# Optimization experiments

Measured on AMD Instinct MI355X. Metric: run time of the kernel, lower is better.

The kernel has to match this reference:

```python
import jax, jax.numpy as jnp
import numpy as np

B, S, E, H = 4, 1024, 1024, 16
D = E // H          # head_dim = 64
ROT = 32            # rotary dims (first ROT channels of each head)


def _rope(x, freqs):
    # x: [B, H, S, D]; freqs: [1, 1, S, ROT]
    r = freqs.shape[-1]
    xl, xr = x[..., :r], x[..., r:]
    half = r // 2
    rot = jnp.concatenate([-xl[..., half:], xl[..., :half]], axis=-1)  # rotate_half
    xl = xl * jnp.cos(freqs) + rot * jnp.sin(freqs)
    return jnp.concatenate([xl, xr], axis=-1)


def setup_inputs() -> dict:
    key = jax.random.key(0)
    ks = jax.random.split(key, 7)
    std = 0.02
    return {
        "hidden_states": jax.random.normal(ks[0], (B, S, E), jnp.float32),
        "rotary_pos_emb": jax.random.normal(ks[1], (1, S, ROT), jnp.float32),
        "q_w": jax.random.normal(ks[2], (E, E), jnp.float32) * std,
        "k_w": jax.random.normal(ks[3], (E, E), jnp.float32) * std,
        "v_w": jax.random.normal(ks[4], (E, E), jnp.float32) * std,
        "o_w": jax.random.normal(ks[5], (E, E), jnp.float32) * std,
        "o_b": jnp.zeros((E,), jnp.float32),
    }


def reference(hidden_states, rotary_pos_emb, q_w, k_w, v_w, o_w, o_b):
    bsz, tgt_len, embed_dim = hidden_states.shape
    scale = D ** -0.5

    def shape(t):  # [B, S, E] -> [B, H, S, D]
        return t.reshape(bsz, tgt_len, H, D).transpose(0, 2, 1, 3)

    q = shape(hidden_states @ q_w.T * scale)
    k = shape(hidden_states @ k_w.T)
    v = shape(hidden_states @ v_w.T)

    freqs = rotary_pos_emb[:, None, :, :]  # [1, 1, S, ROT]
    q = _rope(q, freqs)
    k = _rope(k, freqs)
    v = _rope(v, freqs)

    attn = jnp.einsum("bhqd,bhkd->bhqk", q, k)
    causal = jnp.tril(jnp.ones((tgt_len, tgt_len), bool))
    attn = jnp.where(causal, attn, jnp.finfo(attn.dtype).min)
    attn = jax.nn.softmax(attn, axis=-1)

    out = jnp.einsum("bhqk,bhkd->bhqd", attn, v)
    out = out.transpose(0, 2, 1, 3).reshape(bsz, tgt_len, embed_dim)
    return out @ o_w.T + o_b
```

## Files before the change

### kernel.cpp

```cpp
#include <hip/hip_runtime.h>
#include <hip/hip_bf16.h>

typedef __bf16 bf16;
typedef __attribute__((ext_vector_type(2))) __bf16 bf16x2;
typedef __attribute__((ext_vector_type(4))) __bf16 bf16x4;
typedef __attribute__((ext_vector_type(8))) __bf16 bf16x8;
typedef __attribute__((ext_vector_type(4))) float f32x4;

#define NB 4
#define NS 1024
#define NE 1024
#define NH 16
#define ND 64
#define NROT 32
#define NM (NB*NS)

__device__ __forceinline__ void gload_lds16(const bf16* g, void* l) {
  __builtin_amdgcn_global_load_lds(
      (const __attribute__((address_space(1))) unsigned int*)g,
      (__attribute__((address_space(3))) unsigned int*)l,
      16, 0, 0);
}

struct PrepArgs {
  const float* w0; const float* w1; const float* w2; const float* w3;
  bf16* b0; bf16* b1; bf16* b2; bf16* b3;
  const float* hs; bf16* hb;
  const float* rot; float* ct; float* st;
};
__global__ void k_prep(PrepArgs a) {
  const int y = blockIdx.y;
  const int i = blockIdx.x * 256 + threadIdx.x;
  if (y < 4) {
    const float* s = (y == 0) ? a.w0 : (y == 1) ? a.w1 : (y == 2) ? a.w2 : a.w3;
    bf16* d = (y == 0) ? a.b0 : (y == 1) ? a.b1 : (y == 2) ? a.b2 : a.b3;
    float4 v = reinterpret_cast<const float4*>(s)[i];
    bf16x4 o = { (bf16)v.x, (bf16)v.y, (bf16)v.z, (bf16)v.w };
    *reinterpret_cast<bf16x4*>(d + (size_t)i * 4) = o;
  } else if (y < 8) {
    size_t off = (size_t)(y - 4) * (NM * NE / 16);
    float4 v = reinterpret_cast<const float4*>(a.hs)[off + i];
    bf16x4 o = { (bf16)v.x, (bf16)v.y, (bf16)v.z, (bf16)v.w };
    *reinterpret_cast<bf16x4*>(a.hb + (off + i) * 4) = o;
  } else {
    if (i < NS * NROT) {
      float v = a.rot[i];
      a.ct[i] = cosf(v);
      a.st[i] = sinf(v);
    }
  }
}

template<int BM, int BN, bool SWAP>
__device__ __forceinline__ void gemm_core(
    const bf16* __restrict__ A, const bf16* __restrict__ W,
    bf16* lA, bf16* lB, int m0, int n0, f32x4 (&acc)[BM/32][BN/32])
{
  const int tid = threadIdx.x;
  const int wave = tid >> 6, lane = tid & 63;
  const int wm = wave >> 1, wn = wave & 1;
  const int fr = lane & 15, kg = lane >> 4;

  const int sline = lane >> 3;
  const int lsl   = (lane & 7) ^ sline;
  const int srow  = 2 * sline + (lsl >> 2);
  const int skcol = (lsl & 3) * 8;
  constexpr int ACH = BM / 64;
  constexpr int BCH = BN / 64;
  constexpr int NSTAGE = ACH + BCH;

  auto stage = [&](int kt, int c) {
#pragma unroll
    for (int i = 0; i < ACH; ++i) {
      int chunk = i * 4 + wave;
      gload_lds16(A + (size_t)(m0 + chunk * 16 + srow) * NE + kt + skcol,
                  (char*)lA + c * (BM * 64) + chunk * 1024);
    }
#pragma unroll
    for (int i = 0; i < BCH; ++i) {
      int chunk = i * 4 + wave;
      gload_lds16(W + (size_t)(n0 + chunk * 16 + srow) * NE + kt + skcol,
                  (char*)lB + c * (BN * 64) + chunk * 1024);
    }
  };

  auto foff = [&](int ra) {
    return (ra >> 1) * 128 + (((((ra & 1) << 2) + kg) ^ ((ra >> 1) & 7)) << 4);
  };

  stage(0, 0);

  for (int kt = 0; kt < NE / 32; ++kt) {
    const int c = kt & 1;
    if (kt + 1 < NE / 32) {
      stage((kt + 1) * 32, c ^ 1);
      asm volatile("s_waitcnt vmcnt(%0)\n\ts_barrier" :: "n"(NSTAGE) : "memory");
    } else {
      asm volatile("s_waitcnt vmcnt(0)\n\ts_barrier" ::: "memory");
    }

    const char* cA = (const char*)lA + c * (BM * 64);
    const char* cB = (const char*)lB + c * (BN * 64);
    bf16x8 af[BM / 32], bfr[BN / 32];
#pragma unroll
    for (int i = 0; i < BM / 32; ++i)
      af[i] = *reinterpret_cast<const bf16x8*>(cA + foff(wm * (BM / 2) + i * 16 + fr));
#pragma unroll
    for (int j = 0; j < BN / 32; ++j)
      bfr[j] = *reinterpret_cast<const bf16x8*>(cB + foff(wn * (BN / 2) + j * 16 + fr));
#pragma unroll
    for (int i = 0; i < BM / 32; ++i)
#pragma unroll
      for (int j = 0; j < BN / 32; ++j) {
        if constexpr (SWAP)
          acc[j][i] = __builtin_amdgcn_mfma_f32_16x16x32_bf16(bfr[j], af[i], acc[j][i], 0, 0, 0);
        else
          acc[i][j] = __builtin_amdgcn_mfma_f32_16x16x32_bf16(af[i], bfr[j], acc[i][j], 0, 0, 0);
      }
    asm volatile("s_waitcnt lgkmcnt(0)\n\ts_barrier" ::: "memory");
  }
}

__global__ __launch_bounds__(256) void k_proj(
    const bf16* __restrict__ A, const bf16* __restrict__ Wq, const bf16* __restrict__ Wk,
    const bf16* __restrict__ Wv, bf16* __restrict__ Oq, bf16* __restrict__ Ok,
    bf16* __restrict__ vt, const float* __restrict__ ct, const float* __restrict__ st)
{
  __shared__ bf16 lA[2 * 128 * 32];
  __shared__ bf16 lB[2 * 128 * 32];
  const int z = blockIdx.z;
  const int m0 = blockIdx.x * 128, n0 = blockIdx.y * 128;
  const int tid = threadIdx.x;
  const int wave = tid >> 6, lane = tid & 63;
  const int wm = wave >> 1, wn = wave & 1;
  const int fr = lane & 15, kg = lane >> 4;

  if (z == 2) {
    f32x4 acc[4][4] = {};
    gemm_core<128, 128, true>(A, Wv, lA, lB, m0, n0, acc);

    const int b = m0 >> 10;
    const int h = (n0 + wn * 64) >> 6;
    bf16* vtb = vt + ((size_t)(b * 16 + h)) * ND * NS;
#pragma unroll
    for (int i = 0; i < 4; ++i) {
      int sl = (m0 & (NS - 1)) + wm * 64 + i * 16 + fr;
#pragma unroll
      for (int r = 0; r < 4; ++r) {
        int dbase = kg * 4 + r;
        float x0 = acc[0][i][r];
        float x1 = acc[1][i][r];
        float c0 = ct[sl * NROT + dbase],      sn0 = st[sl * NROT + dbase];
        float c1 = ct[sl * NROT + 16 + dbase], sn1 = st[sl * NROT + 16 + dbase];
        float y0 = x0 * c0 - x1 * sn0;
        float y1 = x1 * c1 + x0 * sn1;
        vtb[(size_t)(dbase)      * NS + sl] = (bf16)y0;
        vtb[(size_t)(16 + dbase) * NS + sl] = (bf16)y1;
        vtb[(size_t)(32 + dbase) * NS + sl] = (bf16)acc[2][i][r];
        vtb[(size_t)(48 + dbase) * NS + sl] = (bf16)acc[3][i][r];
      }
    }
  } else {
    const bf16* W = (z == 0) ? Wq : Wk;
    bf16* Og = (z == 0) ? Oq : Ok;
    const float scale = (z == 0) ? 0.125f * 1.44269504f : 1.0f;

    f32x4 acc[4][4] = {};
    gemm_core<128, 128, false>(A, W, lA, lB, m0, n0, acc);

#pragma unroll
    for (int i = 0; i < 4; ++i) {
      int rowbase = m0 + wm * 64 + i * 16 + kg * 4;
#pragma unroll
      for (int r = 0; r < 4; ++r) {
        int gm = rowbase + r;
        int s = gm & (NS - 1);
        float x0 = acc[i][0][r] * scale;
        float x1 = acc[i][1][r] * scale;
        float c0 = ct[s * NROT + fr],      sn0 = st[s * NROT + fr];
        float c1 = ct[s * NROT + 16 + fr], sn1 = st[s * NROT + 16 + fr];
        float y0 = x0 * c0 - x1 * sn0;
        float y1 = x1 * c1 + x0 * sn1;
        size_t rb = (size_t)gm * NE + n0 + wn * 64;
        Og[rb + 0 * 16 + fr] = (bf16)y0;
        Og[rb + 1 * 16 + fr] = (bf16)y1;
        Og[rb + 2 * 16 + fr] = (bf16)(acc[i][2][r] * scale);
        Og[rb + 3 * 16 + fr] = (bf16)(acc[i][3][r] * scale);
      }
    }
  }
}

__global__ __launch_bounds__(256) void k_gemm_o(
    const bf16* __restrict__ A, const bf16* __restrict__ W, float* __restrict__ Og,
    const float* __restrict__ bias)
{
  __shared__ bf16 lA[2 * 64 * 32];
  __shared__ bf16 lB[2 * 128 * 32];
  const int m0 = blockIdx.x * 64, n0 = blockIdx.y * 128;
  f32x4 acc[2][4] = {};
  gemm_core<64, 128, false>(A, W, lA, lB, m0, n0, acc);

  const int tid = threadIdx.x;
  const int wave = tid >> 6, lane = tid & 63;
  const int wm = wave >> 1, wn = wave & 1;
  const int fr = lane & 15, kg = lane >> 4;
#pragma unroll
  for (int i = 0; i < 2; ++i)
#pragma unroll
    for (int j = 0; j < 4; ++j) {
      int gc = n0 + wn * 64 + j * 16 + fr;
      float bv = bias[gc];
#pragma unroll
      for (int r = 0; r < 4; ++r) {
        int gm = m0 + wm * 32 + i * 16 + kg * 4 + r;
        Og[(size_t)gm * NE + gc] = acc[i][j][r] + bv;
      }
    }
}

__global__ __launch_bounds__(256) void k_attn(
    const bf16* __restrict__ Q, const bf16* __restrict__ K,
    const bf16* __restrict__ VT, bf16* __restrict__ O)
{
  __shared__ bf16 lK[2][64 * 64];
  __shared__ bf16 lVT[64 * 64];
  __shared__ bf16 lP[4][16 * 68];
  const int tid = threadIdx.x;
  const int wave = tid >> 6, lane = tid & 63;
  const int fr = lane & 15, kg = lane >> 4;

  const int qt = 15 - (blockIdx.y >> 3);
  const int bh = blockIdx.x | ((blockIdx.y & 7) << 3);
  const int b = bh >> 4, h = bh & 15;
  const int nt = qt + 1;
  const bf16* Qb  = Q + (size_t)b * NS * NE + h * 64;
  const bf16* Kb  = K + (size_t)b * NS * NE + h * 64;
  const bf16* VTb = VT + (size_t)bh * ND * NS;
  bf16* Ob = O + (size_t)b * NS * NE + h * 64;

  const int qrow0 = qt * 64 + wave * 16;

  bf16x8 qf[2];
#pragma unroll
  for (int kk = 0; kk < 2; ++kk)
    qf[kk] = *reinterpret_cast<const bf16x8*>(
        Qb + (size_t)(qrow0 + fr) * NE + kk * 32 + kg * 8);

  const int srow = lane >> 3;
  const int sslot = (lane & 7) ^ srow;
  const int r0 = wave * 8 + srow;
  const int r1 = (wave + 4) * 8 + srow;
  const bf16* kA0 = Kb + (size_t)r0 * NE + sslot * 8;
  const bf16* kA1 = Kb + (size_t)r1 * NE + sslot * 8;
  const bf16* vA0 = VTb + (size_t)r0 * NS + sslot * 8;
  const bf16* vA1 = VTb + (size_t)r1 * NS + sslot * 8;
  char* ldsKa[2] = { (char*)lK[0] + wave * 1024, (char*)lK[1] + wave * 1024 };
  char* ldsKb[2] = { (char*)lK[0] + (wave + 4) * 1024, (char*)lK[1] + (wave + 4) * 1024 };
  char* ldsVa  = (char*)lVT + wave * 1024;
  char* ldsVb  = (char*)lVT + (wave + 4) * 1024;

  float m_ = -3.0e38f, l_ = 0.f;
  f32x4 oacc[4] = {};

  gload_lds16(kA0, ldsKa[0]);
  gload_lds16(kA1, ldsKb[0]);
  __syncthreads();

  for (int t = 0; t < nt; ++t) {
    const int c = t & 1;
    gload_lds16(vA0 + t * 64, ldsVa);
    gload_lds16(vA1 + t * 64, ldsVb);
    if (t + 1 < nt) {
      gload_lds16(kA0 + (size_t)(t + 1) * 64 * NE, ldsKa[c ^ 1]);
      gload_lds16(kA1 + (size_t)(t + 1) * 64 * NE, ldsKb[c ^ 1]);
    }

    const bf16* lKc = lK[c];
    f32x4 sacc[4] = {};
    __builtin_amdgcn_s_setprio(1);
#pragma unroll
    for (int kk = 0; kk < 2; ++kk)
#pragma unroll
      for (int j = 0; j < 4; ++j) {
        int rc = j * 16 + fr;
        bf16x8 kf = *reinterpret_cast<const bf16x8*>(
            lKc + rc * 64 + (((kg + 4 * kk) ^ (rc & 7)) << 3));
        sacc[j] = __builtin_amdgcn_mfma_f32_16x16x32_bf16(kf, qf[kk], sacc[j], 0, 0, 0);
      }
    __builtin_amdgcn_s_setprio(0);

    if (t == qt) {
      const int ql = wave * 16 + fr;
#pragma unroll
      for (int j = 0; j < 4; ++j)
#pragma unroll
        for (int r = 0; r < 4; ++r)
          if (16 * j + 4 * kg + r > ql) sacc[j][r] = -3.0e38f;
    }

    float m4 = fmaxf(fmaxf(fmaxf(sacc[0][0], sacc[0][1]), fmaxf(sacc[0][2], sacc[0][3])),
                     fmaxf(fmaxf(sacc[1][0], sacc[1][1]), fmaxf(sacc[1][2], sacc[1][3])));
    m4 = fmaxf(m4, fmaxf(fmaxf(fmaxf(sacc[2][0], sacc[2][1]), fmaxf(sacc[2][2], sacc[2][3])),
                         fmaxf(fmaxf(sacc[3][0], sacc[3][1]), fmaxf(sacc[3][2], sacc[3][3]))));
    m4 = fmaxf(m4, __shfl_xor(m4, 16));
    m4 = fmaxf(m4, __shfl_xor(m4, 32));

    if (!__all(m4 - m_ <= 8.0f)) {
      float nm = fmaxf(m_, m4);
      float corr = exp2f(m_ - nm);
      m_ = nm;
      l_ *= corr;
#pragma unroll
      for (int r = 0; r < 4; ++r) {
        float cr = __shfl(corr, kg * 4 + r);
#pragma unroll
        for (int df = 0; df < 4; ++df) oacc[df][r] *= cr;
      }
    }

    float ps = 0.f;
#pragma unroll
    for (int j = 0; j < 4; ++j) {
      float p0 = exp2f(sacc[j][0] - m_);
      float p1 = exp2f(sacc[j][1] - m_);
      float p2 = exp2f(sacc[j][2] - m_);
      float p3 = exp2f(sacc[j][3] - m_);
      ps += (p0 + p1) + (p2 + p3);
      bf16x4 pp = { (bf16)p0, (bf16)p1, (bf16)p2, (bf16)p3 };
      *reinterpret_cast<bf16x4*>(&lP[wave][fr * 68 + j * 16 + kg * 4]) = pp;
    }
    ps += __shfl_xor(ps, 16);
    ps += __shfl_xor(ps, 32);
    l_ += ps;

    __syncthreads();

    __builtin_amdgcn_s_setprio(1);
#pragma unroll
    for (int ks = 0; ks < 2; ++ks) {
      bf16x8 pf = *reinterpret_cast<const bf16x8*>(&lP[wave][fr * 68 + ks * 32 + kg * 8]);
#pragma unroll
      for (int df = 0; df < 4; ++df) {
        int d = df * 16 + fr;
        bf16x8 vf = *reinterpret_cast<const bf16x8*>(
            (const bf16*)lVT + d * 64 + (((kg + 4 * ks) ^ (d & 7)) << 3));
        oacc[df] = __builtin_amdgcn_mfma_f32_16x16x32_bf16(pf, vf, oacc[df], 0, 0, 0);
      }
    }
    __builtin_amdgcn_s_setprio(0);

    __syncthreads();
  }

  float linv[4];
#pragma unroll
  for (int r = 0; r < 4; ++r) linv[r] = 1.0f / __shfl(l_, kg * 4 + r);
#pragma unroll
  for (int df = 0; df < 4; ++df)
#pragma unroll
    for (int r = 0; r < 4; ++r)
      Ob[(size_t)(qrow0 + kg * 4 + r) * NE + df * 16 + fr] = (bf16)(oacc[df][r] * linv[r]);
}

extern "C" void kernel_launch(void* const* d_in, const int* in_sizes, int n_in,
                              void* d_out, int out_size, void* d_ws, size_t ws_size,
                              hipStream_t stream) {
  const float* hs  = (const float*)d_in[0];
  const float* rot = (const float*)d_in[1];
  const float* qw  = (const float*)d_in[2];
  const float* kw  = (const float*)d_in[3];
  const float* vw  = (const float*)d_in[4];
  const float* ow  = (const float*)d_in[5];
  const float* obb = (const float*)d_in[6];
  float* out = (float*)d_out;

  char* ws = (char*)d_ws;
  size_t off = 0;
  bf16* hb  = (bf16*)(ws + off); off += (size_t)NM * NE * 2;
  bf16* wqb = (bf16*)(ws + off); off += (size_t)NE * NE * 2;
  bf16* wkb = (bf16*)(ws + off); off += (size_t)NE * NE * 2;
  bf16* wvb = (bf16*)(ws + off); off += (size_t)NE * NE * 2;
  bf16* wob = (bf16*)(ws + off); off += (size_t)NE * NE * 2;
  bf16* qb  = (bf16*)(ws + off); off += (size_t)NM * NE * 2;
  bf16* kb  = (bf16*)(ws + off); off += (size_t)NM * NE * 2;
  bf16* vt  = (bf16*)(ws + off); off += (size_t)NM * NE * 2;
  float* ct = (float*)(ws + off); off += (size_t)NS * NROT * 4;
  float* st = (float*)(ws + off); off += (size_t)NS * NROT * 4;
  bf16* aob = hb;

  PrepArgs pa = { qw, kw, vw, ow, wqb, wkb, wvb, wob, hs, hb, rot, ct, st };
  k_prep<<<dim3(NE * NE / 4 / 256, 9), dim3(256), 0, stream>>>(pa);

  k_proj<<<dim3(NM / 128, NE / 128, 3), dim3(256), 0, stream>>>(
      hb, wqb, wkb, wvb, qb, kb, vt, ct, st);

  k_attn<<<dim3(8, 128), dim3(256), 0, stream>>>(qb, kb, vt, aob);

  k_gemm_o<<<dim3(NM / 64, NE / 128), dim3(256), 0, stream>>>(aob, wob, out, obb);

  (void)in_sizes; (void)n_in; (void)out_size; (void)ws_size;
}
```

Before: 111.7 us.

## Use 256x256 tiles with 8 waves and BK=64 in QKV projection GEMM

Rewrites the QKV projection kernel to use a 256x256 output tile, 512 threads (8 waves in a 2x4 layout), and a K-step of 64 with an XOR-swizzled LDS layout. Each wave now computes a 128x64 sub-tile with 32 accumulators, which raises arithmetic intensity per LDS and global load. The cost is more registers, 128KB of LDS per block, and a grid of only 192 blocks, which may underfill the 256 CUs.

```diff
diff --git a/kernel.cpp b/kernel.cpp
--- a/kernel.cpp
+++ b/kernel.cpp
@@ -51,7 +51,141 @@
   }
 }
 
-template<int BM, int BN, bool SWAP>
+template<bool SWAP>
+__device__ __forceinline__ void gemm_core256(
+    const bf16* __restrict__ A, const bf16* __restrict__ W,
+    bf16* lA, bf16* lB, int m0, int n0, f32x4 (&acc)[32])
+{
+  const int tid = threadIdx.x;
+  const int wave = tid >> 6, lane = tid & 63;
+  const int wm = wave >> 2, wn = wave & 3;
+  const int fr = lane & 15, kg = lane >> 4;
+  const int lrow8 = lane >> 3, lslot = lane & 7;
+
+  auto stage = [&](int kt, int c) {
+#pragma unroll
+    for (int i = 0; i < 4; ++i) {
+      int chunk = i * 8 + wave;
+      int row = (chunk << 3) + lrow8;
+      int slot = lslot ^ (row & 7);
+      gload_lds16(A + (size_t)(m0 + row) * NE + kt + slot * 8,
+                  (char*)lA + c * 32768 + chunk * 1024);
+      gload_lds16(W + (size_t)(n0 + row) * NE + kt + slot * 8,
+                  (char*)lB + c * 32768 + chunk * 1024);
+    }
+  };
+
+  stage(0, 0);
+
+  for (int kt = 0; kt < NE / 64; ++kt) {
+    const int c = kt & 1;
+    if (kt + 1 < NE / 64) {
+      stage((kt + 1) * 64, c ^ 1);
+      asm volatile("s_waitcnt vmcnt(8)\n\ts_barrier" ::: "memory");
+    } else {
+      asm volatile("s_waitcnt vmcnt(0)\n\ts_barrier" ::: "memory");
+    }
+
+    const char* cA = (const char*)lA + c * 32768;
+    const char* cB = (const char*)lB + c * 32768;
+#pragma unroll
+    for (int kk = 0; kk < 2; ++kk) {
+      bf16x8 af[8], bfr[4];
+#pragma unroll
+      for (int i = 0; i < 8; ++i) {
+        int ra = wm * 128 + i * 16 + fr;
+        af[i] = *reinterpret_cast<const bf16x8*>(cA + ra * 128 + (((kg + 4 * kk) ^ (ra & 7)) << 4));
+      }
+#pragma unroll
+      for (int j = 0; j < 4; ++j) {
+        int rb = wn * 64 + j * 16 + fr;
+        bfr[j] = *reinterpret_cast<const bf16x8*>(cB + rb * 128 + (((kg + 4 * kk) ^ (rb & 7)) << 4));
+      }
+#pragma unroll
+      for (int i = 0; i < 8; ++i)
+#pragma unroll
+        for (int j = 0; j < 4; ++j) {
+          if constexpr (SWAP)
+            acc[j * 8 + i] = __builtin_amdgcn_mfma_f32_16x16x32_bf16(bfr[j], af[i], acc[j * 8 + i], 0, 0, 0);
+          else
+            acc[i * 4 + j] = __builtin_amdgcn_mfma_f32_16x16x32_bf16(af[i], bfr[j], acc[i * 4 + j], 0, 0, 0);
+        }
+    }
+    asm volatile("s_waitcnt lgkmcnt(0)\n\ts_barrier" ::: "memory");
+  }
+}
+
+__global__ __launch_bounds__(512, 2) void k_proj(
+    const bf16* __restrict__ A, const bf16* __restrict__ Wq, const bf16* __restrict__ Wk,
+    const bf16* __restrict__ Wv, bf16* __restrict__ Oq, bf16* __restrict__ Ok,
+    bf16* __restrict__ vt, const float* __restrict__ ct, const float* __restrict__ st)
+{
+  __shared__ bf16 lA[2 * 256 * 64];
+  __shared__ bf16 lB[2 * 256 * 64];
+  const int z = blockIdx.z;
+  const int m0 = blockIdx.x * 256, n0 = blockIdx.y * 256;
+  const int tid = threadIdx.x;
+  const int wave = tid >> 6, lane = tid & 63;
+  const int wm = wave >> 2, wn = wave & 3;
+  const int fr = lane & 15, kg = lane >> 4;
+
+  f32x4 acc[32] = {};
+
+  if (z == 2) {
+    gemm_core256<true>(A, Wv, lA, lB, m0, n0, acc);
+
+    const int b = m0 >> 10;
+    const int h = (n0 + wn * 64) >> 6;
+    bf16* vtb = vt + ((size_t)(b * 16 + h)) * ND * NS;
+#pragma unroll
+    for (int i = 0; i < 8; ++i) {
+      int sl = (m0 & (NS - 1)) + wm * 128 + i * 16 + fr;
+#pragma unroll
+      for (int r = 0; r < 4; ++r) {
+        int dbase = kg * 4 + r;
+        float x0 = acc[0 * 8 + i][r];
+        float x1 = acc[1 * 8 + i][r];
+        float c0 = ct[sl * NROT + dbase],      sn0 = st[sl * NROT + dbase];
+        float c1 = ct[sl * NROT + 16 + dbase], sn1 = st[sl * NROT + 16 + dbase];
+        float y0 = x0 * c0 - x1 * sn0;
+        float y1 = x1 * c1 + x0 * sn1;
+        vtb[(size_t)(dbase)      * NS + sl] = (bf16)y0;
+        vtb[(size_t)(16 + dbase) * NS + sl] = (bf16)y1;
+        vtb[(size_t)(32 + dbase) * NS + sl] = (bf16)acc[2 * 8 + i][r];
+        vtb[(size_t)(48 + dbase) * NS + sl] = (bf16)acc[3 * 8 + i][r];
+      }
+    }
+  } else {
+    const bf16* W = (z == 0) ? Wq : Wk;
+    bf16* Og = (z == 0) ? Oq : Ok;
+    const float scale = (z == 0) ? 0.125f * 1.44269504f : 1.0f;
+
+    gemm_core256<false>(A, W, lA, lB, m0, n0, acc);
+
+#pragma unroll
+    for (int i = 0; i < 8; ++i) {
+      int rowbase = m0 + wm * 128 + i * 16 + kg * 4;
+#pragma unroll
+      for (int r = 0; r < 4; ++r) {
+        int gm = rowbase + r;
+        int s = gm & (NS - 1);
+        float x0 = acc[i * 4 + 0][r] * scale;
+        float x1 = acc[i * 4 + 1][r] * scale;
+        float c0 = ct[s * NROT + fr],      sn0 = st[s * NROT + fr];
+        float c1 = ct[s * NROT + 16 + fr], sn1 = st[s * NROT + 16 + fr];
+        float y0 = x0 * c0 - x1 * sn0;
+        float y1 = x1 * c1 + x0 * sn1;
+        size_t rb = (size_t)gm * NE + n0 + wn * 64;
+        Og[rb + 0 * 16 + fr] = (bf16)y0;
+        Og[rb + 1 * 16 + fr] = (bf16)y1;
+        Og[rb + 2 * 16 + fr] = (bf16)(acc[i * 4 + 2][r] * scale);
+        Og[rb + 3 * 16 + fr] = (bf16)(acc[i * 4 + 3][r] * scale);
+      }
+    }
+  }
+}
+
+template<int BM, int BN>
 __device__ __forceinline__ void gemm_core(
     const bf16* __restrict__ A, const bf16* __restrict__ W,
     bf16* lA, bf16* lB, int m0, int n0, f32x4 (&acc)[BM/32][BN/32])
@@ -111,83 +245,9 @@
 #pragma unroll
     for (int i = 0; i < BM / 32; ++i)
 #pragma unroll
-      for (int j = 0; j < BN / 32; ++j) {
-        if constexpr (SWAP)
-          acc[j][i] = __builtin_amdgcn_mfma_f32_16x16x32_bf16(bfr[j], af[i], acc[j][i], 0, 0, 0);
-        else
-          acc[i][j] = __builtin_amdgcn_mfma_f32_16x16x32_bf16(af[i], bfr[j], acc[i][j], 0, 0, 0);
-      }
+      for (int j = 0; j < BN / 32; ++j)
+        acc[i][j] = __builtin_amdgcn_mfma_f32_16x16x32_bf16(af[i], bfr[j], acc[i][j], 0, 0, 0);
     asm volatile("s_waitcnt lgkmcnt(0)\n\ts_barrier" ::: "memory");
-  }
-}
-
-__global__ __launch_bounds__(256) void k_proj(
-    const bf16* __restrict__ A, const bf16* __restrict__ Wq, const bf16* __restrict__ Wk,
-    const bf16* __restrict__ Wv, bf16* __restrict__ Oq, bf16* __restrict__ Ok,
-    bf16* __restrict__ vt, const float* __restrict__ ct, const float* __restrict__ st)
-{
-  __shared__ bf16 lA[2 * 128 * 32];
-  __shared__ bf16 lB[2 * 128 * 32];
-  const int z = blockIdx.z;
-  const int m0 = blockIdx.x * 128, n0 = blockIdx.y * 128;
-  const int tid = threadIdx.x;
-  const int wave = tid >> 6, lane = tid & 63;
-  const int wm = wave >> 1, wn = wave & 1;
-  const int fr = lane & 15, kg = lane >> 4;
-
-  if (z == 2) {
-    f32x4 acc[4][4] = {};
-    gemm_core<128, 128, true>(A, Wv, lA, lB, m0, n0, acc);
-
-    const int b = m0 >> 10;
-    const int h = (n0 + wn * 64) >> 6;
-    bf16* vtb = vt + ((size_t)(b * 16 + h)) * ND * NS;
-#pragma unroll
-    for (int i = 0; i < 4; ++i) {
-      int sl = (m0 & (NS - 1)) + wm * 64 + i * 16 + fr;
-#pragma unroll
-      for (int r = 0; r < 4; ++r) {
-        int dbase = kg * 4 + r;
-        float x0 = acc[0][i][r];
-        float x1 = acc[1][i][r];
-        float c0 = ct[sl * NROT + dbase],      sn0 = st[sl * NROT + dbase];
-        float c1 = ct[sl * NROT + 16 + dbase], sn1 = st[sl * NROT + 16 + dbase];
-        float y0 = x0 * c0 - x1 * sn0;
-        float y1 = x1 * c1 + x0 * sn1;
-        vtb[(size_t)(dbase)      * NS + sl] = (bf16)y0;
-        vtb[(size_t)(16 + dbase) * NS + sl] = (bf16)y1;
-        vtb[(size_t)(32 + dbase) * NS + sl] = (bf16)acc[2][i][r];
-        vtb[(size_t)(48 + dbase) * NS + sl] = (bf16)acc[3][i][r];
-      }
-    }
-  } else {
-    const bf16* W = (z == 0) ? Wq : Wk;
-    bf16* Og = (z == 0) ? Oq : Ok;
-    const float scale = (z == 0) ? 0.125f * 1.44269504f : 1.0f;
-
-    f32x4 acc[4][4] = {};
-    gemm_core<128, 128, false>(A, W, lA, lB, m0, n0, acc);
-
-#pragma unroll
-    for (int i = 0; i < 4; ++i) {
-      int rowbase = m0 + wm * 64 + i * 16 + kg * 4;
-#pragma unroll
-      for (int r = 0; r < 4; ++r) {
-        int gm = rowbase + r;
-        int s = gm & (NS - 1);
-        float x0 = acc[i][0][r] * scale;
-        float x1 = acc[i][1][r] * scale;
-        float c0 = ct[s * NROT + fr],      sn0 = st[s * NROT + fr];
-        float c1 = ct[s * NROT + 16 + fr], sn1 = st[s * NROT + 16 + fr];
-        float y0 = x0 * c0 - x1 * sn0;
-        float y1 = x1 * c1 + x0 * sn1;
-        size_t rb = (size_t)gm * NE + n0 + wn * 64;
-        Og[rb + 0 * 16 + fr] = (bf16)y0;
-        Og[rb + 1 * 16 + fr] = (bf16)y1;
-        Og[rb + 2 * 16 + fr] = (bf16)(acc[i][2][r] * scale);
-        Og[rb + 3 * 16 + fr] = (bf16)(acc[i][3][r] * scale);
-      }
-    }
   }
 }
 
@@ -199,7 +259,7 @@
   __shared__ bf16 lB[2 * 128 * 32];
   const int m0 = blockIdx.x * 64, n0 = blockIdx.y * 128;
   f32x4 acc[2][4] = {};
-  gemm_core<64, 128, false>(A, W, lA, lB, m0, n0, acc);
+  gemm_core<64, 128>(A, W, lA, lB, m0, n0, acc);
 
   const int tid = threadIdx.x;
   const int wave = tid >> 6, lane = tid & 63;
@@ -392,7 +452,7 @@
   PrepArgs pa = { qw, kw, vw, ow, wqb, wkb, wvb, wob, hs, hb, rot, ct, st };
   k_prep<<<dim3(NE * NE / 4 / 256, 9), dim3(256), 0, stream>>>(pa);
 
-  k_proj<<<dim3(NM / 128, NE / 128, 3), dim3(256), 0, stream>>>(
+  k_proj<<<dim3(NM / 256, NE / 256, 3), dim3(512), 0, stream>>>(
       hb, wqb, wkb, wvb, qb, kb, vt, ct, st);
 
   k_attn<<<dim3(8, 128), dim3(256), 0, stream>>>(qb, kb, vt, aob);
```

After: 105.3 us. 1.06x faster.
